# Kernel optimization log

Measured on AMD Instinct MI355X. Metric: run time of the kernel, lower is better.

## Reference

```python
import jax, jax.numpy as jnp
import numpy as np

M, K, N = 8192, 4096, 4096  # tokens, in_features, out_features


def setup_inputs() -> dict:
    key = jax.random.key(0)
    k1, k2, k3, k4, k5, k6 = jax.random.split(key, 6)
    return {
        "x_q": jax.random.randint(k1, (M, K), 0, 256, dtype=jnp.int32),
        "weight_int8": jax.random.randint(k2, (N, K), 0, 256, dtype=jnp.int32),
        "weight_scale": jax.random.uniform(k3, (N, 1), dtype=jnp.float32) * 0.01 + 1e-4,
        "weight_zero_point": jax.random.randint(k4, (N, 1), 0, 256, dtype=jnp.int32),
        "bias": jax.random.normal(k5, (N,), dtype=jnp.float32),
        "input_scale": jax.random.uniform(k6, (1,), dtype=jnp.float32) * 0.05 + 1e-4,
        "input_zero_point": 128,
    }


def reference(x_q, weight_int8, weight_scale, weight_zero_point, bias, input_scale, input_zero_point):
    # zero-point-subtracted fp32 operands (simulated int32 accumulation in fp32)
    x_f = x_q.astype(jnp.float32) - jnp.float32(input_zero_point)      # [M, K]
    w_f = weight_int8.astype(jnp.float32) - weight_zero_point.astype(jnp.float32)  # [N, K]
    acc = jnp.einsum('mk,nk->mn', x_f, w_f)                            # [M, N]
    dequant_scale = input_scale * weight_scale.T                       # [1, N]
    return acc * dequant_scale + bias                                  # [M, N]
```

## Files before the change

kernel.cpp:

```cpp
#include <hip/hip_runtime.h>
#include <hip/hip_bf16.h>
#include <stdint.h>

typedef int v4i __attribute__((ext_vector_type(4)));

#define AS_GLOBAL(p) ((const __attribute__((address_space(1))) void*)(p))
#define AS_LDS(p)    ((__attribute__((address_space(3))) void*)(p))

__global__ __launch_bounds__(256) void prep_x_kernel(const int* __restrict__ x,
                                                     const int* __restrict__ izp_p,
                                                     signed char* __restrict__ xs,
                                                     int* __restrict__ rowsum, int K) {
    int row = blockIdx.x;
    int izp = izp_p[0];
    const int4* xr = (const int4*)(x + (long)row * K);
    uint32_t* xo = (uint32_t*)(xs + (long)row * K);
    int sum = 0;
    int n4 = K >> 2;
    for (int i = threadIdx.x; i < n4; i += 256) {
        int4 v = xr[i];
        int a0 = v.x - izp, a1 = v.y - izp, a2 = v.z - izp, a3 = v.w - izp;
        sum += a0 + a1 + a2 + a3;
        xo[i] = (uint32_t)(a0 & 0xFF) | ((uint32_t)(a1 & 0xFF) << 8) |
                ((uint32_t)(a2 & 0xFF) << 16) | ((uint32_t)(a3 & 0xFF) << 24);
    }
    sum += __shfl_down(sum, 32);
    sum += __shfl_down(sum, 16);
    sum += __shfl_down(sum, 8);
    sum += __shfl_down(sum, 4);
    sum += __shfl_down(sum, 2);
    sum += __shfl_down(sum, 1);
    __shared__ int red[4];
    if ((threadIdx.x & 63) == 0) red[threadIdx.x >> 6] = sum;
    __syncthreads();
    if (threadIdx.x == 0) rowsum[row] = red[0] + red[1] + red[2] + red[3];
}

__global__ __launch_bounds__(256) void prep_w_kernel(const int* __restrict__ w,
                                                     signed char* __restrict__ ws, int K) {
    int row = blockIdx.x;
    const int4* wr = (const int4*)(w + (long)row * K);
    uint32_t* wo = (uint32_t*)(ws + (long)row * K);
    int n4 = K >> 2;
    for (int i = threadIdx.x; i < n4; i += 256) {
        int4 v = wr[i];
        int a0 = v.x - 128, a1 = v.y - 128, a2 = v.z - 128, a3 = v.w - 128;
        wo[i] = (uint32_t)(a0 & 0xFF) | ((uint32_t)(a1 & 0xFF) << 8) |
                ((uint32_t)(a2 & 0xFF) << 16) | ((uint32_t)(a3 & 0xFF) << 24);
    }
}


#define BAR  __builtin_amdgcn_s_barrier()
#define LGKM0 asm volatile("s_waitcnt lgkmcnt(0)" ::: "memory")
#define VM4  asm volatile("s_waitcnt vmcnt(4)" ::: "memory")
#define PRIO1 __builtin_amdgcn_s_setprio(1)
#define PRIO0 __builtin_amdgcn_s_setprio(0)

#define STAGE(gbase, opofs, half, buf, tile) do {                                     \
    int t_ = (tile); if (t_ >= NT) t_ -= NT;                                          \
    const signed char* src_ = (gbase) + (long)((half) * 128) * K + (long)t_ * 128;    \
    signed char* dst_ = ldsw + (buf) * 65536 + (opofs) + (half) * 16384;              \
    __builtin_amdgcn_global_load_lds(AS_GLOBAL(src_), AS_LDS(dst_), 16, 0, 0);        \
    __builtin_amdgcn_global_load_lds(AS_GLOBAL(src_ + 64L * K), AS_LDS(dst_ + 8192), 16, 0, 0); \
  } while (0)

#define READ_A(buf, mi) do {                                                          \
    af[mi][0] = *(const v4i*)(lds + (buf) * 65536 + aoff0 + (mi) * 2048);             \
    af[mi][1] = *(const v4i*)(lds + (buf) * 65536 + aoff1 + (mi) * 2048); } while (0)
#define READ_B(buf, ni) do {                                                          \
    bf[ni][0] = *(const v4i*)(lds + (buf) * 65536 + boff0 + (ni) * 2048);             \
    bf[ni][1] = *(const v4i*)(lds + (buf) * 65536 + boff1 + (ni) * 2048); } while (0)

#define MFMA_1(mi, ni, ks)                                                             \
    acc[mi][ni] = __builtin_amdgcn_mfma_i32_16x16x64_i8(af[mi][ks], bf[ni][ks], acc[mi][ni], 0, 0, 0);

#define MFMAQ(mb, nb) do {                                                             \
    MFMA_1(mb + 0, nb + 0, 0) MFMA_1(mb + 0, nb + 1, 0)                                \
    MFMA_1(mb + 1, nb + 0, 0) MFMA_1(mb + 1, nb + 1, 0)                                \
    MFMA_1(mb + 2, nb + 0, 0) MFMA_1(mb + 2, nb + 1, 0)                                \
    MFMA_1(mb + 3, nb + 0, 0) MFMA_1(mb + 3, nb + 1, 0)                                \
    MFMA_1(mb + 0, nb + 0, 1) MFMA_1(mb + 0, nb + 1, 1)                                \
    MFMA_1(mb + 1, nb + 0, 1) MFMA_1(mb + 1, nb + 1, 1)                                \
    MFMA_1(mb + 2, nb + 0, 1) MFMA_1(mb + 2, nb + 1, 1)                                \
    MFMA_1(mb + 3, nb + 0, 1) MFMA_1(mb + 3, nb + 1, 1) } while (0)

#define KTILE(b, tA, tB) do {                                                          \
                                                                    \
    READ_A(b, 0); READ_A(b, 1); READ_B(b, 0); READ_B(b, 1);                            \
    READ_A(b, 2); READ_A(b, 3);                                                        \
    STAGE(gA, 0, 0, (b) ^ 1, tA);                                                      \
    PRIO1; MFMAQ(0, 0); PRIO0;                                                         \
    LGKM0; BAR;                                                                        \
                                                                     \
    READ_B(b, 2); READ_B(b, 3);                                                        \
    STAGE(gA, 0, 1, (b) ^ 1, tA);                                                      \
    PRIO1; MFMAQ(0, 2); PRIO0;                                                         \
    LGKM0; BAR;                                                                        \
                                                                     \
    READ_A(b, 4); READ_A(b, 5); READ_A(b, 6); READ_A(b, 7);                            \
    STAGE(gB, 32768, 0, (b), tB);                                                      \
    PRIO1; MFMAQ(4, 0); PRIO0;                                                         \
    LGKM0; BAR;                                                                        \
                                                                    \
    STAGE(gB, 32768, 1, (b), tB);                                                      \
    PRIO1; MFMAQ(4, 2); PRIO0;                                                         \
    VM4; LGKM0; BAR;                                                                   \
  } while (0)

__global__ __launch_bounds__(512, 2) void gemm_i8_8ph(
    const signed char* __restrict__ A,
    const signed char* __restrict__ B,
    const int* __restrict__ rowsum, const float* __restrict__ wscale,
    const int* __restrict__ wzp, const float* __restrict__ bias,
    const float* __restrict__ iscale, float* __restrict__ C,
    int M, int N, int K) {
  __shared__ signed char lds[131072];
  const int tid = threadIdx.x;
  const int w = tid >> 6, l = tid & 63;
  const int wm = w >> 2, wn = w & 3;
  const int fr = l & 15, fq = l >> 4;

  int nwg = gridDim.x, bid = blockIdx.x;
  if ((nwg & 7) == 0) { int cpx = nwg >> 3; bid = (bid & 7) * cpx + (bid >> 3); }
  const int ntiles = N >> 8;
  const int mt = bid / ntiles, nt = bid - mt * ntiles;
  const long brow = (long)mt << 8, bcol = (long)nt << 8;

  const int NT = K >> 7;
  const int NI = NT >> 1;

  const int srow = w * 8 + (l >> 3);
  const int schunk = ((l & 7) ^ (l >> 3)) << 4;
  const signed char* gA = A + (brow + srow) * (long)K + schunk;
  const signed char* gB = B + (bcol + srow) * (long)K + schunk;
  signed char* ldsw = lds + w * 1024;

  const int axor = fr & 7;
  const int aoff0 = (wm * 128 + fr) * 128 + ((fq ^ axor) << 4);
  const int aoff1 = (wm * 128 + fr) * 128 + (((4 + fq) ^ axor) << 4);
  const int boff0 = 32768 + (wn * 64 + fr) * 128 + ((fq ^ axor) << 4);
  const int boff1 = 32768 + (wn * 64 + fr) * 128 + (((4 + fq) ^ axor) << 4);

  v4i acc[8][4] = {};
  v4i af[8][2], bf[4][2];

  STAGE(gB, 32768, 0, 0, 0); STAGE(gB, 32768, 1, 0, 0);
  STAGE(gA, 0, 0, 0, 0);     STAGE(gA, 0, 1, 0, 0);
  STAGE(gB, 32768, 0, 1, 1); STAGE(gB, 32768, 1, 1, 1);
  VM4; BAR;

  for (int i = 0; i < NI; ++i) {
    const int t1 = 2 * i + 1, t2 = 2 * i + 2, t3 = 2 * i + 3;
    KTILE(0, t1, t2);
    KTILE(1, t2, t3);
  }

  const float is = iscale[0];
  int rs[8][4];
#pragma unroll
  for (int mi = 0; mi < 8; ++mi)
#pragma unroll
    for (int j = 0; j < 4; ++j)
      rs[mi][j] = rowsum[(int)brow + wm * 128 + mi * 16 + fq * 4 + j];
#pragma unroll
  for (int ni = 0; ni < 4; ++ni) {
    const int col = (int)bcol + wn * 64 + ni * 16 + fr;
    const float sc = is * wscale[col];
    const int zpc = 128 - wzp[col];
    const float bi = bias[col];
#pragma unroll
    for (int mi = 0; mi < 8; ++mi) {
      const int row0 = (int)brow + wm * 128 + mi * 16 + fq * 4;
#pragma unroll
      for (int j = 0; j < 4; ++j) {
        const int v = acc[mi][ni][j] + zpc * rs[mi][j];
        C[(long)(row0 + j) * N + col] = (float)v * sc + bi;
      }
    }
  }
}

extern "C" void kernel_launch(void* const* d_in, const int* in_sizes, int n_in,
                              void* d_out, int out_size, void* d_ws, size_t ws_size,
                              hipStream_t stream) {
    const int* x_q = (const int*)d_in[0];
    const int* w_q = (const int*)d_in[1];
    const float* wscale = (const float*)d_in[2];
    const int* wzp = (const int*)d_in[3];
    const float* bias = (const float*)d_in[4];
    const float* iscale = (const float*)d_in[5];
    const int* izp = (const int*)d_in[6];

    int N = in_sizes[2];
    int K = in_sizes[1] / N;
    int M = in_sizes[0] / K;

    signed char* xs = (signed char*)d_ws;
    signed char* wsq = xs + (size_t)M * K;
    int* rowsum = (int*)(wsq + (size_t)N * K);

    prep_x_kernel<<<M, 256, 0, stream>>>(x_q, izp, xs, rowsum, K);
    prep_w_kernel<<<N, 256, 0, stream>>>(w_q, wsq, K);

    int grid = (M / 256) * (N / 256);
    gemm_i8_8ph<<<grid, 512, 0, stream>>>(xs, wsq, rowsum, wscale, wzp, bias, iscale,
                                          (float*)d_out, M, N, K);
}
```

Measured before the change: 189.5 us.

## Merge prep kernels and restructure GEMM k-tile into two phases

The separate x and weight prep kernels are merged into one launch covering M+N blocks, which removes a kernel launch and its tail. The GEMM k-tile loop drops from four barrier-separated phases to two. Each phase loads four A fragments into a reduced register buffer (afs[4][2] instead of af[8][2]) and issues 32 MFMAs between barriers. This halves the barriers per k-tile and lowers register pressure. In exchange, LDS reads and global-to-LDS stages are bunched together, so they interleave less finely with the MFMAs.

Measured after the change: 186.5 us. No clear change (-1.6%).

```diff
diff --git a/kernel.cpp b/kernel.cpp
--- a/kernel.cpp
+++ b/kernel.cpp
@@ -7,46 +7,46 @@
 #define AS_GLOBAL(p) ((const __attribute__((address_space(1))) void*)(p))
 #define AS_LDS(p)    ((__attribute__((address_space(3))) void*)(p))
 
-__global__ __launch_bounds__(256) void prep_x_kernel(const int* __restrict__ x,
-                                                     const int* __restrict__ izp_p,
-                                                     signed char* __restrict__ xs,
-                                                     int* __restrict__ rowsum, int K) {
+__global__ __launch_bounds__(256) void prep_kernel(const int* __restrict__ x,
+                                                   const int* __restrict__ w,
+                                                   const int* __restrict__ izp_p,
+                                                   signed char* __restrict__ xs,
+                                                   signed char* __restrict__ wsq,
+                                                   int* __restrict__ rowsum, int M, int K) {
     int row = blockIdx.x;
-    int izp = izp_p[0];
-    const int4* xr = (const int4*)(x + (long)row * K);
-    uint32_t* xo = (uint32_t*)(xs + (long)row * K);
-    int sum = 0;
     int n4 = K >> 2;
-    for (int i = threadIdx.x; i < n4; i += 256) {
-        int4 v = xr[i];
-        int a0 = v.x - izp, a1 = v.y - izp, a2 = v.z - izp, a3 = v.w - izp;
-        sum += a0 + a1 + a2 + a3;
-        xo[i] = (uint32_t)(a0 & 0xFF) | ((uint32_t)(a1 & 0xFF) << 8) |
-                ((uint32_t)(a2 & 0xFF) << 16) | ((uint32_t)(a3 & 0xFF) << 24);
-    }
-    sum += __shfl_down(sum, 32);
-    sum += __shfl_down(sum, 16);
-    sum += __shfl_down(sum, 8);
-    sum += __shfl_down(sum, 4);
-    sum += __shfl_down(sum, 2);
-    sum += __shfl_down(sum, 1);
-    __shared__ int red[4];
-    if ((threadIdx.x & 63) == 0) red[threadIdx.x >> 6] = sum;
-    __syncthreads();
-    if (threadIdx.x == 0) rowsum[row] = red[0] + red[1] + red[2] + red[3];
-}
-
-__global__ __launch_bounds__(256) void prep_w_kernel(const int* __restrict__ w,
-                                                     signed char* __restrict__ ws, int K) {
-    int row = blockIdx.x;
-    const int4* wr = (const int4*)(w + (long)row * K);
-    uint32_t* wo = (uint32_t*)(ws + (long)row * K);
-    int n4 = K >> 2;
-    for (int i = threadIdx.x; i < n4; i += 256) {
-        int4 v = wr[i];
-        int a0 = v.x - 128, a1 = v.y - 128, a2 = v.z - 128, a3 = v.w - 128;
-        wo[i] = (uint32_t)(a0 & 0xFF) | ((uint32_t)(a1 & 0xFF) << 8) |
-                ((uint32_t)(a2 & 0xFF) << 16) | ((uint32_t)(a3 & 0xFF) << 24);
+    if (row < M) {
+        int izp = izp_p[0];
+        const int4* xr = (const int4*)(x + (long)row * K);
+        uint32_t* xo = (uint32_t*)(xs + (long)row * K);
+        int sum = 0;
+        for (int i = threadIdx.x; i < n4; i += 256) {
+            int4 v = xr[i];
+            int a0 = v.x - izp, a1 = v.y - izp, a2 = v.z - izp, a3 = v.w - izp;
+            sum += a0 + a1 + a2 + a3;
+            xo[i] = (uint32_t)(a0 & 0xFF) | ((uint32_t)(a1 & 0xFF) << 8) |
+                    ((uint32_t)(a2 & 0xFF) << 16) | ((uint32_t)(a3 & 0xFF) << 24);
+        }
+        sum += __shfl_down(sum, 32);
+        sum += __shfl_down(sum, 16);
+        sum += __shfl_down(sum, 8);
+        sum += __shfl_down(sum, 4);
+        sum += __shfl_down(sum, 2);
+        sum += __shfl_down(sum, 1);
+        __shared__ int red[4];
+        if ((threadIdx.x & 63) == 0) red[threadIdx.x >> 6] = sum;
+        __syncthreads();
+        if (threadIdx.x == 0) rowsum[row] = red[0] + red[1] + red[2] + red[3];
+    } else {
+        int wrow = row - M;
+        const int4* wr = (const int4*)(w + (long)wrow * K);
+        uint32_t* wo = (uint32_t*)(wsq + (long)wrow * K);
+        for (int i = threadIdx.x; i < n4; i += 256) {
+            int4 v = wr[i];
+            int a0 = v.x - 128, a1 = v.y - 128, a2 = v.z - 128, a3 = v.w - 128;
+            wo[i] = (uint32_t)(a0 & 0xFF) | ((uint32_t)(a1 & 0xFF) << 8) |
+                    ((uint32_t)(a2 & 0xFF) << 16) | ((uint32_t)(a3 & 0xFF) << 24);
+        }
     }
 }
 
@@ -65,46 +65,38 @@
     __builtin_amdgcn_global_load_lds(AS_GLOBAL(src_ + 64L * K), AS_LDS(dst_ + 8192), 16, 0, 0); \
   } while (0)
 
-#define READ_A(buf, mi) do {                                                          \
-    af[mi][0] = *(const v4i*)(lds + (buf) * 65536 + aoff0 + (mi) * 2048);             \
-    af[mi][1] = *(const v4i*)(lds + (buf) * 65536 + aoff1 + (mi) * 2048); } while (0)
+#define READ_AS(buf, s, mi) do {                                                      \
+    afs[s][0] = *(const v4i*)(lds + (buf) * 65536 + aoff0 + (mi) * 2048);             \
+    afs[s][1] = *(const v4i*)(lds + (buf) * 65536 + aoff1 + (mi) * 2048); } while (0)
 #define READ_B(buf, ni) do {                                                          \
     bf[ni][0] = *(const v4i*)(lds + (buf) * 65536 + boff0 + (ni) * 2048);             \
     bf[ni][1] = *(const v4i*)(lds + (buf) * 65536 + boff1 + (ni) * 2048); } while (0)
 
-#define MFMA_1(mi, ni, ks)                                                             \
-    acc[mi][ni] = __builtin_amdgcn_mfma_i32_16x16x64_i8(af[mi][ks], bf[ni][ks], acc[mi][ni], 0, 0, 0);
-
-#define MFMAQ(mb, nb) do {                                                             \
-    MFMA_1(mb + 0, nb + 0, 0) MFMA_1(mb + 0, nb + 1, 0)                                \
-    MFMA_1(mb + 1, nb + 0, 0) MFMA_1(mb + 1, nb + 1, 0)                                \
-    MFMA_1(mb + 2, nb + 0, 0) MFMA_1(mb + 2, nb + 1, 0)                                \
-    MFMA_1(mb + 3, nb + 0, 0) MFMA_1(mb + 3, nb + 1, 0)                                \
-    MFMA_1(mb + 0, nb + 0, 1) MFMA_1(mb + 0, nb + 1, 1)                                \
-    MFMA_1(mb + 1, nb + 0, 1) MFMA_1(mb + 1, nb + 1, 1)                                \
-    MFMA_1(mb + 2, nb + 0, 1) MFMA_1(mb + 2, nb + 1, 1)                                \
-    MFMA_1(mb + 3, nb + 0, 1) MFMA_1(mb + 3, nb + 1, 1) } while (0)
+#define M1(s, mi, ni, ks)                                                              \
+    acc[mi][ni] = __builtin_amdgcn_mfma_i32_16x16x64_i8(afs[s][ks], bf[ni][ks], acc[mi][ni], 0, 0, 0);
+
+#define MFMA32(mb) do {                                                                \
+    M1(0, mb + 0, 0, 0) M1(0, mb + 0, 1, 0) M1(1, mb + 1, 0, 0) M1(1, mb + 1, 1, 0)   \
+    M1(2, mb + 2, 0, 0) M1(2, mb + 2, 1, 0) M1(3, mb + 3, 0, 0) M1(3, mb + 3, 1, 0)   \
+    M1(0, mb + 0, 2, 0) M1(0, mb + 0, 3, 0) M1(1, mb + 1, 2, 0) M1(1, mb + 1, 3, 0)   \
+    M1(2, mb + 2, 2, 0) M1(2, mb + 2, 3, 0) M1(3, mb + 3, 2, 0) M1(3, mb + 3, 3, 0)   \
+    M1(0, mb + 0, 0, 1) M1(0, mb + 0, 1, 1) M1(1, mb + 1, 0, 1) M1(1, mb + 1, 1, 1)   \
+    M1(2, mb + 2, 0, 1) M1(2, mb + 2, 1, 1) M1(3, mb + 3, 0, 1) M1(3, mb + 3, 1, 1)   \
+    M1(0, mb + 0, 2, 1) M1(0, mb + 0, 3, 1) M1(1, mb + 1, 2, 1) M1(1, mb + 1, 3, 1)   \
+    M1(2, mb + 2, 2, 1) M1(2, mb + 2, 3, 1) M1(3, mb + 3, 2, 1) M1(3, mb + 3, 3, 1)   \
+  } while (0)
 
 #define KTILE(b, tA, tB) do {                                                          \
-                                                                    \
-    READ_A(b, 0); READ_A(b, 1); READ_B(b, 0); READ_B(b, 1);                            \
-    READ_A(b, 2); READ_A(b, 3);                                                        \
-    STAGE(gA, 0, 0, (b) ^ 1, tA);                                                      \
-    PRIO1; MFMAQ(0, 0); PRIO0;                                                         \
+              \
+    READ_AS(b, 0, 0); READ_AS(b, 1, 1); READ_AS(b, 2, 2); READ_AS(b, 3, 3);            \
+    READ_B(b, 0); READ_B(b, 1); READ_B(b, 2); READ_B(b, 3);                            \
+    STAGE(gA, 0, 0, (b) ^ 1, tA); STAGE(gA, 0, 1, (b) ^ 1, tA);                        \
+    PRIO1; MFMA32(0); PRIO0;                                                           \
     LGKM0; BAR;                                                                        \
-                                                                     \
-    READ_B(b, 2); READ_B(b, 3);                                                        \
-    STAGE(gA, 0, 1, (b) ^ 1, tA);                                                      \
-    PRIO1; MFMAQ(0, 2); PRIO0;                                                         \
-    LGKM0; BAR;                                                                        \
-                                                                     \
-    READ_A(b, 4); READ_A(b, 5); READ_A(b, 6); READ_A(b, 7);                            \
-    STAGE(gB, 32768, 0, (b), tB);                                                      \
-    PRIO1; MFMAQ(4, 0); PRIO0;                                                         \
-    LGKM0; BAR;                                                                        \
-                                                                    \
-    STAGE(gB, 32768, 1, (b), tB);                                                      \
-    PRIO1; MFMAQ(4, 2); PRIO0;                                                         \
+                    \
+    READ_AS(b, 0, 4); READ_AS(b, 1, 5); READ_AS(b, 2, 6); READ_AS(b, 3, 7);            \
+    STAGE(gB, 32768, 0, (b), tB); STAGE(gB, 32768, 1, (b), tB);                        \
+    PRIO1; MFMA32(4); PRIO0;                                                           \
     VM4; LGKM0; BAR;                                                                   \
   } while (0)
 
@@ -143,7 +135,7 @@
   const int boff1 = 32768 + (wn * 64 + fr) * 128 + (((4 + fq) ^ axor) << 4);
 
   v4i acc[8][4] = {};
-  v4i af[8][2], bf[4][2];
+  v4i afs[4][2], bf[4][2];
 
   STAGE(gB, 32768, 0, 0, 0); STAGE(gB, 32768, 1, 0, 0);
   STAGE(gA, 0, 0, 0, 0);     STAGE(gA, 0, 1, 0, 0);
@@ -200,8 +192,7 @@
     signed char* wsq = xs + (size_t)M * K;
     int* rowsum = (int*)(wsq + (size_t)N * K);
 
-    prep_x_kernel<<<M, 256, 0, stream>>>(x_q, izp, xs, rowsum, K);
-    prep_w_kernel<<<N, 256, 0, stream>>>(w_q, wsq, K);
+    prep_kernel<<<M + N, 256, 0, stream>>>(x_q, w_q, izp, xs, wsq, rowsum, M, K);
 
     int grid = (M / 256) * (N / 256);
     gemm_i8_8ph<<<grid, 512, 0, stream>>>(xs, wsq, rowsum, wscale, wzp, bias, iscale,
```
